# Performance work log

Measured on AMD Instinct MI355X. Metric: run time of the kernel, lower is better.

## Reference

```python
import jax, jax.numpy as jnp
import numpy as np

N_SEQ, BS, E, H = 2048, 8, 512, 8
HD = E // H  # 64


def setup_inputs() -> dict:
    key = jax.random.key(0)
    k1, k2, k3 = jax.random.split(key, 3)
    seq = jax.random.normal(k1, (N_SEQ, BS, E), dtype=jnp.float32)
    # xavier_uniform for Linear(E, 3E): bound = sqrt(6/(fan_in+fan_out))
    b_qkv_w = float(np.sqrt(6.0 / (E + 3 * E)))
    W_qkv = jax.random.uniform(k2, (3 * E, E), minval=-b_qkv_w, maxval=b_qkv_w, dtype=jnp.float32)
    b_out_w = float(np.sqrt(6.0 / (E + E)))
    W_out = jax.random.uniform(k3, (E, E), minval=-b_out_w, maxval=b_out_w, dtype=jnp.float32)
    b_qkv = jnp.zeros((3 * E,), dtype=jnp.float32)
    b_out = jnp.zeros((E,), dtype=jnp.float32)
    return {"seq": seq, "W_qkv": W_qkv, "b_qkv": b_qkv, "W_out": W_out, "b_out": b_out}


def reference(seq, W_qkv, b_qkv, W_out, b_out):
    n, bs, e = seq.shape
    # fused QKV projection: [n, bs, 3E]
    qkv = jnp.einsum('nbe,fe->nbf', seq, W_qkv) + b_qkv
    # [n, bs, 3, H, HD] -> q/k/v each [n, bs*H, HD] (bs outer, H inner)
    qkv = qkv.reshape(n, bs, 3, H, HD)
    q = qkv[:, :, 0].reshape(n, bs * H, HD)
    k = qkv[:, :, 1].reshape(n, bs * H, HD)
    v = qkv[:, :, 2].reshape(n, bs * H, HD)
    scale = 1.0 / jnp.sqrt(jnp.asarray(HD, dtype=seq.dtype))
    # full [bs*H, n, n] score matrix as in the original
    attn = jnp.einsum('qbd,kbd->bqk', q * scale, k)
    attn = jax.nn.softmax(attn, axis=-1)
    out = jnp.einsum('bqk,kbd->qbd', attn, v)  # [n, bs*H, HD]
    out = out.reshape(n, bs, e)
    return jnp.einsum('nbe,fe->nbf', out, W_out) + b_out
```

## Files before the change

kernel.cpp:

```cpp
#include <hip/hip_runtime.h>
#include <stdint.h>

typedef unsigned short ushort_t;
typedef unsigned int uint32;
typedef __attribute__((ext_vector_type(8))) short short8;
typedef __attribute__((ext_vector_type(4))) float f32x4;
typedef __attribute__((ext_vector_type(16))) float f32x16;
typedef __attribute__((ext_vector_type(4))) uint32 uint4v;

#define NSEQ 2048
#define BSZ 8
#define EMB 512
#define NHEAD 8
#define HDIM 64
#define MTOK (NSEQ*BSZ)
#define NH_TOT (BSZ*NHEAD)
#define NT (NSEQ/64)

#define VMCNT0 asm volatile("s_waitcnt vmcnt(0)" ::: "memory")
#define VMCNT4 asm volatile("s_waitcnt vmcnt(4)" ::: "memory")
#define BAR __builtin_amdgcn_s_barrier()

__device__ __forceinline__ ushort_t f2bf(float f) {
  uint32_t u = __builtin_bit_cast(uint32_t, f);
  u += 0x7FFFu + ((u >> 16) & 1u);
  return (ushort_t)(u >> 16);
}
__device__ __forceinline__ float bf2f(ushort_t u) {
  uint32_t x = ((uint32_t)u) << 16;
  return __builtin_bit_cast(float, x);
}

__device__ __forceinline__ void gll16(const void* g, void* l) {
  __builtin_amdgcn_global_load_lds(
      (const __attribute__((address_space(1))) void*)g,
      (__attribute__((address_space(3))) void*)l, 16, 0, 0);
}

__device__ __forceinline__ int SW(int r) { return (r & 7) ^ ((r >> 3) & 7); }

__global__ void cvt_f32_bf16(const float* __restrict__ in, ushort_t* __restrict__ out, int n4) {
  int i = blockIdx.x * blockDim.x + threadIdx.x;
  if (i >= n4) return;
  float4 v = reinterpret_cast<const float4*>(in)[i];
  union { ushort_t u[4]; uint64_t q; } o;
  o.u[0] = f2bf(v.x); o.u[1] = f2bf(v.y); o.u[2] = f2bf(v.z); o.u[3] = f2bf(v.w);
  reinterpret_cast<uint64_t*>(out)[i] = o.q;
}

template<int MODE>
__global__ __launch_bounds__(256) void gemm_bt(
    const ushort_t* __restrict__ A, const ushort_t* __restrict__ B,
    const float* __restrict__ bias,
    float* __restrict__ Cf, ushort_t* __restrict__ Cq,
    int M, int N, int K)
{
  __shared__ __align__(16) ushort_t As[128*64];
  __shared__ __align__(16) ushort_t Bs[128*64];
  const int t = threadIdx.x;
  const int w = t >> 6, l = t & 63;
  const int tm = blockIdx.y * 128, tn = blockIdx.x * 128;
  const int wm = w >> 1, wn = w & 1;

  f32x4 acc[4][4] = {};

  for (int k0 = 0; k0 < K; k0 += 64) {
    #pragma unroll
    for (int j = 0; j < 4; ++j) {
      int row = j*32 + w*8 + (l >> 3);
      int cole = ((l & 7) * 8) ^ ((row & 7) << 3);
      const ushort_t* ga = A + (size_t)(tm + row) * K + k0 + cole;
      const ushort_t* gb = B + (size_t)(tn + row) * K + k0 + cole;
      gll16(ga, As + j*2048 + w*512 + l*8);
      gll16(gb, Bs + j*2048 + w*512 + l*8);
    }
    __syncthreads();
    #pragma unroll
    for (int kk = 0; kk < 2; ++kk) {
      short8 af[4], bfr[4];
      #pragma unroll
      for (int mi = 0; mi < 4; ++mi) {
        int row = wm*64 + mi*16 + (l & 15);
        int byte = row*128 + ((kk*64 + ((l >> 4) * 16)) ^ ((row & 7) << 4));
        af[mi] = *reinterpret_cast<const short8*>(reinterpret_cast<const char*>(As) + byte);
      }
      #pragma unroll
      for (int ni = 0; ni < 4; ++ni) {
        int row = wn*64 + ni*16 + (l & 15);
        int byte = row*128 + ((kk*64 + ((l >> 4) * 16)) ^ ((row & 7) << 4));
        bfr[ni] = *reinterpret_cast<const short8*>(reinterpret_cast<const char*>(Bs) + byte);
      }
      #pragma unroll
      for (int mi = 0; mi < 4; ++mi)
        #pragma unroll
        for (int ni = 0; ni < 4; ++ni)
          acc[mi][ni] = __builtin_amdgcn_mfma_f32_16x16x32_bf16(af[mi], bfr[ni], acc[mi][ni], 0, 0, 0);
    }
    __syncthreads();
  }

  #pragma unroll
  for (int mi = 0; mi < 4; ++mi) {
    #pragma unroll
    for (int ni = 0; ni < 4; ++ni) {
      #pragma unroll
      for (int r = 0; r < 4; ++r) {
        int row = tm + wm*64 + mi*16 + ((l >> 4) * 4) + r;
        int col = tn + wn*64 + ni*16 + (l & 15);
        float v = acc[mi][ni][r] + bias[col];
        if constexpr (MODE == 1) {
          Cf[(size_t)row * N + col] = v;
        } else {
          int w3 = col >> 9, hx = (col >> 6) & 7, hd = col & 63;
          int n = row >> 3, bb = row & 7;
          Cq[(size_t)w3 * ((size_t)NH_TOT * NSEQ * HDIM)
             + ((size_t)(bb * NHEAD + hx) * NSEQ + n) * HDIM + hd] = f2bf(v);
        }
      }
    }
  }
}

__global__ __launch_bounds__(256) void transpose_v(
    const ushort_t* __restrict__ V, ushort_t* __restrict__ VT)
{
  __shared__ __align__(16) ushort_t T[64*64];
  const int t = threadIdx.x;
  const int head = blockIdx.y;
  const int n0 = blockIdx.x * 64;
  const size_t base = (size_t)head * NSEQ * HDIM;
  const int r = t >> 3, c0 = (t & 7) * 8;

  short8 a = *reinterpret_cast<const short8*>(V + base + (size_t)(n0 + r) * HDIM + c0);
  short8 b = *reinterpret_cast<const short8*>(V + base + (size_t)(n0 + r + 32) * HDIM + c0);
  #pragma unroll
  for (int e = 0; e < 8; ++e) {
    int d = c0 + e; int sw = SW(d) << 4;
    *reinterpret_cast<ushort_t*>(reinterpret_cast<char*>(T) + d*128 + ((r*2) ^ sw)) = (ushort_t)a[e];
    *reinterpret_cast<ushort_t*>(reinterpret_cast<char*>(T) + d*128 + (((r+32)*2) ^ sw)) = (ushort_t)b[e];
  }
  __syncthreads();
  #pragma unroll
  for (int i = 0; i < 2; ++i) {
    int d = (t >> 3) + 32*i, ch = t & 7;
    short8 v = *reinterpret_cast<const short8*>(
        reinterpret_cast<const char*>(T) + d*128 + ((ch*16) ^ (SW(d) << 4)));
    *reinterpret_cast<short8*>(VT + (size_t)head * HDIM * NSEQ + (size_t)d * NSEQ + n0 + ch*8) = v;
  }
}

#define CSC 0.18033688011112042f

__global__ __launch_bounds__(256, 3) void attn_fwd(
    const ushort_t* __restrict__ Qb, const ushort_t* __restrict__ Kb,
    const ushort_t* __restrict__ VTb, ushort_t* __restrict__ Ob)
{
  __shared__ __align__(16) ushort_t Ks[3][64*64];
  __shared__ __align__(16) ushort_t Vs[3][64*64];
  const int t = threadIdx.x, w = t >> 6, l = t & 63;
  const int lq = l & 31, h = l >> 5;
  const int L = blockIdx.x + 16 * blockIdx.y;
  const int Tid = (L & 7) * 128 + (L >> 3);
  const int bh = Tid >> 4, qt = Tid & 15;
  const int b = bh >> 3, hh = bh & 7;
  const size_t hbase  = (size_t)bh * NSEQ * HDIM;
  const size_t vtbase = (size_t)bh * HDIM * NSEQ;
  const int qbase = qt*128 + w*32;

  short8 qreg[4];
  #pragma unroll
  for (int kd = 0; kd < 4; ++kd) {
    short8 raw = *reinterpret_cast<const short8*>(
        Qb + hbase + (size_t)(qbase + lq) * HDIM + kd*16 + h*8);
    short8 q;
    #pragma unroll
    for (int e = 0; e < 8; ++e)
      q[e] = (short)f2bf(bf2f((ushort_t)raw[e]) * CSC);
    qreg[kd] = q;
  }

  f32x16 Oacc[2] = {};
  f32x16 lacc = {};

  const short ONE = (short)0x3F80;
  short8 ones = { ONE, ONE, ONE, ONE, ONE, ONE, ONE, ONE };

  const int srow = t >> 3;
  const int scol = (t & 7) * 8;
  const int c0 = scol ^ (SW(srow) << 3);
  const int c1 = scol ^ (SW(srow + 32) << 3);
  const ushort_t* Kg0 = Kb  + hbase  + (size_t)srow       * HDIM + c0;
  const ushort_t* Kg1 = Kb  + hbase  + (size_t)(srow+32)  * HDIM + c1;
  const ushort_t* Vg0 = VTb + vtbase + (size_t)srow       * NSEQ + c0;
  const ushort_t* Vg1 = VTb + vtbase + (size_t)(srow+32)  * NSEQ + c1;

  auto STAGE = [&](int bi, int kt) {
    size_t ko = (size_t)kt * 64 * HDIM;
    int    vo = kt * 64;
    gll16(Kg0 + ko, &Ks[bi][0]    + t*8);
    gll16(Kg1 + ko, &Ks[bi][2048] + t*8);
    gll16(Vg0 + vo, &Vs[bi][0]    + t*8);
    gll16(Vg1 + vo, &Vs[bi][2048] + t*8);
  };

  VMCNT0;
  STAGE(0, 0);
  STAGE(1, 1);

  int cur = 0;
  #pragma unroll 1
  for (int kt = 0; kt < NT; ++kt) {
    if (kt + 1 < NT) { VMCNT4; } else { VMCNT0; }
    BAR;
    if (kt + 2 < NT) {
      int sb = cur + 2; if (sb >= 3) sb -= 3;
      STAGE(sb, kt + 2);
    }

    const char* KsC = reinterpret_cast<const char*>(&Ks[cur][0]);
    const char* VsC = reinterpret_cast<const char*>(&Vs[cur][0]);

    short8 kf[2][4];
    #pragma unroll
    for (int rp = 0; rp < 2; ++rp) {
      int row = rp*32 + lq;
      int swr = SW(row) << 4;
      #pragma unroll
      for (int kd = 0; kd < 4; ++kd)
        kf[rp][kd] = *reinterpret_cast<const short8*>(
            KsC + row*128 + ((kd*32 + h*16) ^ swr));
    }

    f32x16 s0 = {}, s1 = {};
    __builtin_amdgcn_s_setprio(1);
    #pragma unroll
    for (int kd = 0; kd < 4; ++kd) {
      s0 = __builtin_amdgcn_mfma_f32_32x32x16_bf16(kf[0][kd], qreg[kd], s0, 0, 0, 0);
      s1 = __builtin_amdgcn_mfma_f32_32x32x16_bf16(kf[1][kd], qreg[kd], s1, 0, 0, 0);
    }
    __builtin_amdgcn_s_setprio(0);

    short8 vf[2][4];
    #pragma unroll
    for (int dt = 0; dt < 2; ++dt) {
      int d = dt*32 + lq;
      int swd = SW(d) << 4;
      #pragma unroll
      for (int km = 0; km < 4; ++km)
        vf[dt][km] = *reinterpret_cast<const short8*>(
            VsC + d*128 + ((km*32 + h*16) ^ swd));
    }

    #pragma unroll
    for (int r = 0; r < 16; ++r) {
      s0[r] = __builtin_amdgcn_exp2f(s0[r]);
      s1[r] = __builtin_amdgcn_exp2f(s1[r]);
    }

    uint32 w0[8], w1[8];
    #pragma unroll
    for (int i = 0; i < 8; ++i) {
      float a0 = s0[2*i], b0 = s0[2*i+1];
      float a1 = s1[2*i], b1 = s1[2*i+1];
      asm("v_cvt_pk_bf16_f32 %0, %1, %2" : "=v"(w0[i]) : "v"(a0), "v"(b0));
      asm("v_cvt_pk_bf16_f32 %0, %1, %2" : "=v"(w1[i]) : "v"(a1), "v"(b1));
    }
    uint32 pa[4][4];
    #pragma unroll
    for (int sg = 0; sg < 2; ++sg) {
      uint32 a, bb;
      a = w0[4*sg+0]; bb = w0[4*sg+2];
      asm("v_permlane32_swap_b32 %0, %1" : "+v"(a), "+v"(bb));
      pa[sg][0] = a; pa[sg][2] = bb;
      a = w0[4*sg+1]; bb = w0[4*sg+3];
      asm("v_permlane32_swap_b32 %0, %1" : "+v"(a), "+v"(bb));
      pa[sg][1] = a; pa[sg][3] = bb;
      a = w1[4*sg+0]; bb = w1[4*sg+2];
      asm("v_permlane32_swap_b32 %0, %1" : "+v"(a), "+v"(bb));
      pa[2+sg][0] = a; pa[2+sg][2] = bb;
      a = w1[4*sg+1]; bb = w1[4*sg+3];
      asm("v_permlane32_swap_b32 %0, %1" : "+v"(a), "+v"(bb));
      pa[2+sg][1] = a; pa[2+sg][3] = bb;
    }

    __builtin_amdgcn_s_setprio(1);
    #pragma unroll
    for (int km = 0; km < 4; ++km) {
      uint4v u; u[0] = pa[km][0]; u[1] = pa[km][1]; u[2] = pa[km][2]; u[3] = pa[km][3];
      short8 paf = __builtin_bit_cast(short8, u);
      Oacc[0] = __builtin_amdgcn_mfma_f32_32x32x16_bf16(paf, vf[0][km], Oacc[0], 0, 0, 0);
      Oacc[1] = __builtin_amdgcn_mfma_f32_32x32x16_bf16(paf, vf[1][km], Oacc[1], 0, 0, 0);
      lacc    = __builtin_amdgcn_mfma_f32_32x32x16_bf16(paf, ones,     lacc,    0, 0, 0);
    }
    __builtin_amdgcn_s_setprio(0);

    cur = cur + 1; if (cur >= 3) cur = 0;
  }

  #pragma unroll
  for (int r = 0; r < 16; ++r) {
    float li = __builtin_amdgcn_rcpf(lacc[r]);
    int qrow = (r & 3) + 8*(r >> 2) + 4*h;
    int n = qbase + qrow;
    #pragma unroll
    for (int dt = 0; dt < 2; ++dt) {
      int d = dt*32 + lq;
      Ob[((size_t)n * BSZ + b) * EMB + hh*64 + d] = f2bf(Oacc[dt][r] * li);
    }
  }
}

extern "C" void kernel_launch(void* const* d_in, const int* in_sizes, int n_in,
                              void* d_out, int out_size, void* d_ws, size_t ws_size,
                              hipStream_t stream) {
  (void)in_sizes; (void)n_in; (void)out_size; (void)ws_size;
  const float* seq  = (const float*)d_in[0];
  const float* Wqkv = (const float*)d_in[1];
  const float* bqkv = (const float*)d_in[2];
  const float* Wout = (const float*)d_in[3];
  const float* bout = (const float*)d_in[4];
  float* out = (float*)d_out;

  ushort_t* seq_bf  = (ushort_t*)d_ws;
  ushort_t* wqkv_bf = seq_bf  + (size_t)MTOK * EMB;
  ushort_t* wout_bf = wqkv_bf + (size_t)3 * EMB * EMB;
  ushort_t* qkvbuf  = wout_bf + (size_t)EMB * EMB;
  ushort_t* vtbuf   = qkvbuf  + (size_t)3 * NH_TOT * NSEQ * HDIM;
  ushort_t* attno   = qkvbuf  + (size_t)2 * NH_TOT * NSEQ * HDIM;

  cvt_f32_bf16<<<(MTOK*EMB/4 + 255)/256, 256, 0, stream>>>(seq, seq_bf, MTOK*EMB/4);
  cvt_f32_bf16<<<(3*EMB*EMB/4 + 255)/256, 256, 0, stream>>>(Wqkv, wqkv_bf, 3*EMB*EMB/4);
  cvt_f32_bf16<<<(EMB*EMB/4 + 255)/256, 256, 0, stream>>>(Wout, wout_bf, EMB*EMB/4);

  gemm_bt<0><<<dim3(12, 128), 256, 0, stream>>>(seq_bf, wqkv_bf, bqkv, nullptr, qkvbuf,
                                                MTOK, 3*EMB, EMB);

  const ushort_t* Qb  = qkvbuf;
  const ushort_t* Kb  = qkvbuf + (size_t)NH_TOT * NSEQ * HDIM;
  const ushort_t* Vb  = Kb     + (size_t)NH_TOT * NSEQ * HDIM;

  transpose_v<<<dim3(32, 64), 256, 0, stream>>>(Vb, vtbuf);

  attn_fwd<<<dim3(16, 64), 256, 0, stream>>>(Qb, Kb, vtbuf, attno);

  gemm_bt<1><<<dim3(4, 128), 256, 0, stream>>>(attno, wout_bf, bout, out, nullptr,
                                               MTOK, EMB, EMB);
}
```

Measured before the change: 173.5 us.

## Process two query sub-tiles per wave in attention and fuse conversion kernels

Each attention wave now handles 64 query rows (two 32-row sub-tiles) instead of 32, so each K/V tile loaded into LDS and registers is reused twice, and the grid is halved. The row-sum is computed with VALU reductions and a lane shuffle instead of an extra MFMA against a ones vector. The three fp32-to-bf16 conversion launches are merged into one kernel. The cost is higher register pressure, with launch bounds lowered from 3 to 2 blocks per SM, and fewer blocks to fill the GPU.

Measured after the change: 159.3 us. 8.2% less time.

```diff
diff --git a/kernel.cpp b/kernel.cpp
--- a/kernel.cpp
+++ b/kernel.cpp
@@ -5,6 +5,8 @@
 typedef unsigned int uint32;
 typedef __attribute__((ext_vector_type(8))) short short8;
 typedef __attribute__((ext_vector_type(4))) float f32x4;
+typedef __attribute__((ext_vector_type(8))) float f32x8;
+typedef __attribute__((ext_vector_type(2))) float f32x2;
 typedef __attribute__((ext_vector_type(16))) float f32x16;
 typedef __attribute__((ext_vector_type(4))) uint32 uint4v;
 
@@ -39,13 +41,32 @@
 
 __device__ __forceinline__ int SW(int r) { return (r & 7) ^ ((r >> 3) & 7); }
 
-__global__ void cvt_f32_bf16(const float* __restrict__ in, ushort_t* __restrict__ out, int n4) {
+__device__ __forceinline__ float vsum32(f32x16 a, f32x16 b) {
+  f32x16 s = a + b;
+  f32x8 t8 = __builtin_shufflevector(s, s, 0,1,2,3,4,5,6,7)
+           + __builtin_shufflevector(s, s, 8,9,10,11,12,13,14,15);
+  f32x4 t4 = __builtin_shufflevector(t8, t8, 0,1,2,3)
+           + __builtin_shufflevector(t8, t8, 4,5,6,7);
+  f32x2 t2 = __builtin_shufflevector(t4, t4, 0,1)
+           + __builtin_shufflevector(t4, t4, 2,3);
+  return t2[0] + t2[1];
+}
+
+__global__ void cvt3(const float* __restrict__ a, ushort_t* __restrict__ oa, int na4,
+                     const float* __restrict__ b, ushort_t* __restrict__ ob, int nb4,
+                     const float* __restrict__ c, ushort_t* __restrict__ oc, int nc4) {
   int i = blockIdx.x * blockDim.x + threadIdx.x;
-  if (i >= n4) return;
-  float4 v = reinterpret_cast<const float4*>(in)[i];
+  const float* src; ushort_t* dst; int j = i;
+  if (j < na4) { src = a; dst = oa; }
+  else {
+    j -= na4;
+    if (j < nb4) { src = b; dst = ob; }
+    else { j -= nb4; if (j >= nc4) return; src = c; dst = oc; }
+  }
+  float4 v = reinterpret_cast<const float4*>(src)[j];
   union { ushort_t u[4]; uint64_t q; } o;
   o.u[0] = f2bf(v.x); o.u[1] = f2bf(v.y); o.u[2] = f2bf(v.z); o.u[3] = f2bf(v.w);
-  reinterpret_cast<uint64_t*>(out)[i] = o.q;
+  reinterpret_cast<uint64_t*>(dst)[j] = o.q;
 }
 
 template<int MODE>
@@ -151,7 +172,7 @@
 
 #define CSC 0.18033688011112042f
 
-__global__ __launch_bounds__(256, 3) void attn_fwd(
+__global__ __launch_bounds__(256, 2) void attn_fwd(
     const ushort_t* __restrict__ Qb, const ushort_t* __restrict__ Kb,
     const ushort_t* __restrict__ VTb, ushort_t* __restrict__ Ob)
 {
@@ -159,31 +180,30 @@
   __shared__ __align__(16) ushort_t Vs[3][64*64];
   const int t = threadIdx.x, w = t >> 6, l = t & 63;
   const int lq = l & 31, h = l >> 5;
-  const int L = blockIdx.x + 16 * blockIdx.y;
-  const int Tid = (L & 7) * 128 + (L >> 3);
-  const int bh = Tid >> 4, qt = Tid & 15;
+  const int L = blockIdx.x + 8 * blockIdx.y;
+  const int Tid = (L & 7) * 64 + (L >> 3);
+  const int bh = Tid >> 3, qt = Tid & 7;
   const int b = bh >> 3, hh = bh & 7;
   const size_t hbase  = (size_t)bh * NSEQ * HDIM;
   const size_t vtbase = (size_t)bh * HDIM * NSEQ;
-  const int qbase = qt*128 + w*32;
-
-  short8 qreg[4];
+  const int qbase = qt*256 + w*64;
+
+  short8 qreg[2][4];
   #pragma unroll
-  for (int kd = 0; kd < 4; ++kd) {
-    short8 raw = *reinterpret_cast<const short8*>(
-        Qb + hbase + (size_t)(qbase + lq) * HDIM + kd*16 + h*8);
-    short8 q;
-    #pragma unroll
-    for (int e = 0; e < 8; ++e)
-      q[e] = (short)f2bf(bf2f((ushort_t)raw[e]) * CSC);
-    qreg[kd] = q;
-  }
-
-  f32x16 Oacc[2] = {};
-  f32x16 lacc = {};
-
-  const short ONE = (short)0x3F80;
-  short8 ones = { ONE, ONE, ONE, ONE, ONE, ONE, ONE, ONE };
+  for (int qb = 0; qb < 2; ++qb)
+    #pragma unroll
+    for (int kd = 0; kd < 4; ++kd) {
+      short8 raw = *reinterpret_cast<const short8*>(
+          Qb + hbase + (size_t)(qbase + qb*32 + lq) * HDIM + kd*16 + h*8);
+      short8 q;
+      #pragma unroll
+      for (int e = 0; e < 8; ++e)
+        q[e] = (short)f2bf(bf2f((ushort_t)raw[e]) * CSC);
+      qreg[qb][kd] = q;
+    }
+
+  f32x16 Oacc[2][2] = {};
+  float l_run0 = 0.f, l_run1 = 0.f;
 
   const int srow = t >> 3;
   const int scol = (t & 7) * 8;
@@ -231,14 +251,93 @@
             KsC + row*128 + ((kd*32 + h*16) ^ swr));
     }
 
-    f32x16 s0 = {}, s1 = {};
-    __builtin_amdgcn_s_setprio(1);
-    #pragma unroll
-    for (int kd = 0; kd < 4; ++kd) {
-      s0 = __builtin_amdgcn_mfma_f32_32x32x16_bf16(kf[0][kd], qreg[kd], s0, 0, 0, 0);
-      s1 = __builtin_amdgcn_mfma_f32_32x32x16_bf16(kf[1][kd], qreg[kd], s1, 0, 0, 0);
-    }
-    __builtin_amdgcn_s_setprio(0);
+    uint32 pa0[4][4], pa1[4][4];
+
+    {
+      f32x16 s0 = {}, s1 = {};
+      __builtin_amdgcn_s_setprio(1);
+      #pragma unroll
+      for (int kd = 0; kd < 4; ++kd) {
+        s0 = __builtin_amdgcn_mfma_f32_32x32x16_bf16(kf[0][kd], qreg[0][kd], s0, 0, 0, 0);
+        s1 = __builtin_amdgcn_mfma_f32_32x32x16_bf16(kf[1][kd], qreg[0][kd], s1, 0, 0, 0);
+      }
+      __builtin_amdgcn_s_setprio(0);
+      #pragma unroll
+      for (int r = 0; r < 16; ++r) {
+        s0[r] = __builtin_amdgcn_exp2f(s0[r]);
+        s1[r] = __builtin_amdgcn_exp2f(s1[r]);
+      }
+      float ps = vsum32(s0, s1);
+      ps += __shfl_xor(ps, 32);
+      l_run0 += ps;
+      uint32 w0[8], w1[8];
+      #pragma unroll
+      for (int i = 0; i < 8; ++i) {
+        float a0 = s0[2*i], b0 = s0[2*i+1];
+        float a1 = s1[2*i], b1 = s1[2*i+1];
+        asm("v_cvt_pk_bf16_f32 %0, %1, %2" : "=v"(w0[i]) : "v"(a0), "v"(b0));
+        asm("v_cvt_pk_bf16_f32 %0, %1, %2" : "=v"(w1[i]) : "v"(a1), "v"(b1));
+      }
+      #pragma unroll
+      for (int sg = 0; sg < 2; ++sg) {
+        uint32 a, bb;
+        a = w0[4*sg+0]; bb = w0[4*sg+2];
+        asm("v_permlane32_swap_b32 %0, %1" : "+v"(a), "+v"(bb));
+        pa0[sg][0] = a; pa0[sg][2] = bb;
+        a = w0[4*sg+1]; bb = w0[4*sg+3];
+        asm("v_permlane32_swap_b32 %0, %1" : "+v"(a), "+v"(bb));
+        pa0[sg][1] = a; pa0[sg][3] = bb;
+        a = w1[4*sg+0]; bb = w1[4*sg+2];
+        asm("v_permlane32_swap_b32 %0, %1" : "+v"(a), "+v"(bb));
+        pa0[2+sg][0] = a; pa0[2+sg][2] = bb;
+        a = w1[4*sg+1]; bb = w1[4*sg+3];
+        asm("v_permlane32_swap_b32 %0, %1" : "+v"(a), "+v"(bb));
+        pa0[2+sg][1] = a; pa0[2+sg][3] = bb;
+      }
+    }
+
+    {
+      f32x16 s0 = {}, s1 = {};
+      __builtin_amdgcn_s_setprio(1);
+      #pragma unroll
+      for (int kd = 0; kd < 4; ++kd) {
+        s0 = __builtin_amdgcn_mfma_f32_32x32x16_bf16(kf[0][kd], qreg[1][kd], s0, 0, 0, 0);
+        s1 = __builtin_amdgcn_mfma_f32_32x32x16_bf16(kf[1][kd], qreg[1][kd], s1, 0, 0, 0);
+      }
+      __builtin_amdgcn_s_setprio(0);
+      #pragma unroll
+      for (int r = 0; r < 16; ++r) {
+        s0[r] = __builtin_amdgcn_exp2f(s0[r]);
+        s1[r] = __builtin_amdgcn_exp2f(s1[r]);
+      }
+      float ps = vsum32(s0, s1);
+      ps += __shfl_xor(ps, 32);
+      l_run1 += ps;
+      uint32 w0[8], w1[8];
+      #pragma unroll
+      for (int i = 0; i < 8; ++i) {
+        float a0 = s0[2*i], b0 = s0[2*i+1];
+        float a1 = s1[2*i], b1 = s1[2*i+1];
+        asm("v_cvt_pk_bf16_f32 %0, %1, %2" : "=v"(w0[i]) : "v"(a0), "v"(b0));
+        asm("v_cvt_pk_bf16_f32 %0, %1, %2" : "=v"(w1[i]) : "v"(a1), "v"(b1));
+      }
+      #pragma unroll
+      for (int sg = 0; sg < 2; ++sg) {
+        uint32 a, bb;
+        a = w0[4*sg+0]; bb = w0[4*sg+2];
+        asm("v_permlane32_swap_b32 %0, %1" : "+v"(a), "+v"(bb));
+        pa1[sg][0] = a; pa1[sg][2] = bb;
+        a = w0[4*sg+1]; bb = w0[4*sg+3];
+        asm("v_permlane32_swap_b32 %0, %1" : "+v"(a), "+v"(bb));
+        pa1[sg][1] = a; pa1[sg][3] = bb;
+        a = w1[4*sg+0]; bb = w1[4*sg+2];
+        asm("v_permlane32_swap_b32 %0, %1" : "+v"(a), "+v"(bb));
+        pa1[2+sg][0] = a; pa1[2+sg][2] = bb;
+        a = w1[4*sg+1]; bb = w1[4*sg+3];
+        asm("v_permlane32_swap_b32 %0, %1" : "+v"(a), "+v"(bb));
+        pa1[2+sg][1] = a; pa1[2+sg][3] = bb;
+      }
+    }
 
     short8 vf[2][4];
     #pragma unroll
@@ -251,61 +350,37 @@
             VsC + d*128 + ((km*32 + h*16) ^ swd));
     }
 
-    #pragma unroll
-    for (int r = 0; r < 16; ++r) {
-      s0[r] = __builtin_amdgcn_exp2f(s0[r]);
-      s1[r] = __builtin_amdgcn_exp2f(s1[r]);
-    }
-
-    uint32 w0[8], w1[8];
-    #pragma unroll
-    for (int i = 0; i < 8; ++i) {
-      float a0 = s0[2*i], b0 = s0[2*i+1];
-      float a1 = s1[2*i], b1 = s1[2*i+1];
-      asm("v_cvt_pk_bf16_f32 %0, %1, %2" : "=v"(w0[i]) : "v"(a0), "v"(b0));
-      asm("v_cvt_pk_bf16_f32 %0, %1, %2" : "=v"(w1[i]) : "v"(a1), "v"(b1));
-    }
-    uint32 pa[4][4];
-    #pragma unroll
-    for (int sg = 0; sg < 2; ++sg) {
-      uint32 a, bb;
-      a = w0[4*sg+0]; bb = w0[4*sg+2];
-      asm("v_permlane32_swap_b32 %0, %1" : "+v"(a), "+v"(bb));
-      pa[sg][0] = a; pa[sg][2] = bb;
-      a = w0[4*sg+1]; bb = w0[4*sg+3];
-      asm("v_permlane32_swap_b32 %0, %1" : "+v"(a), "+v"(bb));
-      pa[sg][1] = a; pa[sg][3] = bb;
-      a = w1[4*sg+0]; bb = w1[4*sg+2];
-      asm("v_permlane32_swap_b32 %0, %1" : "+v"(a), "+v"(bb));
-      pa[2+sg][0] = a; pa[2+sg][2] = bb;
-      a = w1[4*sg+1]; bb = w1[4*sg+3];
-      asm("v_permlane32_swap_b32 %0, %1" : "+v"(a), "+v"(bb));
-      pa[2+sg][1] = a; pa[2+sg][3] = bb;
-    }
-
     __builtin_amdgcn_s_setprio(1);
     #pragma unroll
     for (int km = 0; km < 4; ++km) {
-      uint4v u; u[0] = pa[km][0]; u[1] = pa[km][1]; u[2] = pa[km][2]; u[3] = pa[km][3];
-      short8 paf = __builtin_bit_cast(short8, u);
-      Oacc[0] = __builtin_amdgcn_mfma_f32_32x32x16_bf16(paf, vf[0][km], Oacc[0], 0, 0, 0);
-      Oacc[1] = __builtin_amdgcn_mfma_f32_32x32x16_bf16(paf, vf[1][km], Oacc[1], 0, 0, 0);
-      lacc    = __builtin_amdgcn_mfma_f32_32x32x16_bf16(paf, ones,     lacc,    0, 0, 0);
+      uint4v u0; u0[0] = pa0[km][0]; u0[1] = pa0[km][1]; u0[2] = pa0[km][2]; u0[3] = pa0[km][3];
+      short8 paf0 = __builtin_bit_cast(short8, u0);
+      uint4v u1; u1[0] = pa1[km][0]; u1[1] = pa1[km][1]; u1[2] = pa1[km][2]; u1[3] = pa1[km][3];
+      short8 paf1 = __builtin_bit_cast(short8, u1);
+      Oacc[0][0] = __builtin_amdgcn_mfma_f32_32x32x16_bf16(paf0, vf[0][km], Oacc[0][0], 0, 0, 0);
+      Oacc[0][1] = __builtin_amdgcn_mfma_f32_32x32x16_bf16(paf0, vf[1][km], Oacc[0][1], 0, 0, 0);
+      Oacc[1][0] = __builtin_amdgcn_mfma_f32_32x32x16_bf16(paf1, vf[0][km], Oacc[1][0], 0, 0, 0);
+      Oacc[1][1] = __builtin_amdgcn_mfma_f32_32x32x16_bf16(paf1, vf[1][km], Oacc[1][1], 0, 0, 0);
     }
     __builtin_amdgcn_s_setprio(0);
 
     cur = cur + 1; if (cur >= 3) cur = 0;
   }
 
+  float linv0 = __builtin_amdgcn_rcpf(l_run0);
+  float linv1 = __builtin_amdgcn_rcpf(l_run1);
   #pragma unroll
   for (int r = 0; r < 16; ++r) {
-    float li = __builtin_amdgcn_rcpf(lacc[r]);
     int qrow = (r & 3) + 8*(r >> 2) + 4*h;
-    int n = qbase + qrow;
+    float li0 = __shfl(linv0, qrow, 64);
+    float li1 = __shfl(linv1, qrow, 64);
     #pragma unroll
     for (int dt = 0; dt < 2; ++dt) {
       int d = dt*32 + lq;
-      Ob[((size_t)n * BSZ + b) * EMB + hh*64 + d] = f2bf(Oacc[dt][r] * li);
+      int n0 = qbase + qrow;
+      int n1 = qbase + 32 + qrow;
+      Ob[((size_t)n0 * BSZ + b) * EMB + hh*64 + d] = f2bf(Oacc[0][dt][r] * li0);
+      Ob[((size_t)n1 * BSZ + b) * EMB + hh*64 + d] = f2bf(Oacc[1][dt][r] * li1);
     }
   }
 }
@@ -328,9 +403,9 @@
   ushort_t* vtbuf   = qkvbuf  + (size_t)3 * NH_TOT * NSEQ * HDIM;
   ushort_t* attno   = qkvbuf  + (size_t)2 * NH_TOT * NSEQ * HDIM;
 
-  cvt_f32_bf16<<<(MTOK*EMB/4 + 255)/256, 256, 0, stream>>>(seq, seq_bf, MTOK*EMB/4);
-  cvt_f32_bf16<<<(3*EMB*EMB/4 + 255)/256, 256, 0, stream>>>(Wqkv, wqkv_bf, 3*EMB*EMB/4);
-  cvt_f32_bf16<<<(EMB*EMB/4 + 255)/256, 256, 0, stream>>>(Wout, wout_bf, EMB*EMB/4);
+  const int na4 = MTOK*EMB/4, nb4 = 3*EMB*EMB/4, nc4 = EMB*EMB/4;
+  cvt3<<<(na4+nb4+nc4 + 255)/256, 256, 0, stream>>>(
+      seq, seq_bf, na4, Wqkv, wqkv_bf, nb4, Wout, wout_bf, nc4);
 
   gemm_bt<0><<<dim3(12, 128), 256, 0, stream>>>(seq_bf, wqkv_bf, bqkv, nullptr, qkvbuf,
                                                 MTOK, 3*EMB, EMB);
@@ -341,7 +416,7 @@
 
   transpose_v<<<dim3(32, 64), 256, 0, stream>>>(Vb, vtbuf);
 
-  attn_fwd<<<dim3(16, 64), 256, 0, stream>>>(Qb, Kb, vtbuf, attno);
+  attn_fwd<<<dim3(8, 64), 256, 0, stream>>>(Qb, Kb, vtbuf, attno);
 
   gemm_bt<1><<<dim3(4, 128), 256, 0, stream>>>(attno, wout_bf, bout, out, nullptr,
                                                MTOK, EMB, EMB);
```

## Drop ones-MFMA row sum, double-buffer attention LDS, fuse conversion kernels

Applied to the files above, without the earlier changes.

In the attention kernel, the row-sum MFMA against a ones vector is replaced by a VALU/shuffle reduction of the exponentiated scores, accumulated as a scalar and broadcast per row at the end. The LDS ring shrinks from triple to double buffering with an extra barrier per iteration, and launch bounds rise to 4 blocks per CU to raise occupancy. The V fragment loads move later to shorten register live ranges, and the three f32->bf16 conversion launches are merged into one. This trades MFMA work and LDS footprint for extra VALU reductions, cross-lane shuffles and a second barrier per tile, which reduces latency hiding.

Result: faster. 165.5 us (-4.6%).

```diff
diff --git a/kernel.cpp b/kernel.cpp
--- a/kernel.cpp
+++ b/kernel.cpp
@@ -5,6 +5,8 @@
 typedef unsigned int uint32;
 typedef __attribute__((ext_vector_type(8))) short short8;
 typedef __attribute__((ext_vector_type(4))) float f32x4;
+typedef __attribute__((ext_vector_type(8))) float f32x8;
+typedef __attribute__((ext_vector_type(2))) float f32x2;
 typedef __attribute__((ext_vector_type(16))) float f32x16;
 typedef __attribute__((ext_vector_type(4))) uint32 uint4v;
 
@@ -39,13 +41,32 @@
 
 __device__ __forceinline__ int SW(int r) { return (r & 7) ^ ((r >> 3) & 7); }
 
-__global__ void cvt_f32_bf16(const float* __restrict__ in, ushort_t* __restrict__ out, int n4) {
+__device__ __forceinline__ float vsum32(f32x16 a, f32x16 b) {
+  f32x16 s = a + b;
+  f32x8 t8 = __builtin_shufflevector(s, s, 0,1,2,3,4,5,6,7)
+           + __builtin_shufflevector(s, s, 8,9,10,11,12,13,14,15);
+  f32x4 t4 = __builtin_shufflevector(t8, t8, 0,1,2,3)
+           + __builtin_shufflevector(t8, t8, 4,5,6,7);
+  f32x2 t2 = __builtin_shufflevector(t4, t4, 0,1)
+           + __builtin_shufflevector(t4, t4, 2,3);
+  return t2[0] + t2[1];
+}
+
+__global__ void cvt3(const float* __restrict__ a, ushort_t* __restrict__ oa, int na4,
+                     const float* __restrict__ b, ushort_t* __restrict__ ob, int nb4,
+                     const float* __restrict__ c, ushort_t* __restrict__ oc, int nc4) {
   int i = blockIdx.x * blockDim.x + threadIdx.x;
-  if (i >= n4) return;
-  float4 v = reinterpret_cast<const float4*>(in)[i];
+  const float* src; ushort_t* dst; int j = i;
+  if (j < na4) { src = a; dst = oa; }
+  else {
+    j -= na4;
+    if (j < nb4) { src = b; dst = ob; }
+    else { j -= nb4; if (j >= nc4) return; src = c; dst = oc; }
+  }
+  float4 v = reinterpret_cast<const float4*>(src)[j];
   union { ushort_t u[4]; uint64_t q; } o;
   o.u[0] = f2bf(v.x); o.u[1] = f2bf(v.y); o.u[2] = f2bf(v.z); o.u[3] = f2bf(v.w);
-  reinterpret_cast<uint64_t*>(out)[i] = o.q;
+  reinterpret_cast<uint64_t*>(dst)[j] = o.q;
 }
 
 template<int MODE>
@@ -151,12 +172,12 @@
 
 #define CSC 0.18033688011112042f
 
-__global__ __launch_bounds__(256, 3) void attn_fwd(
+__global__ __launch_bounds__(256, 4) void attn_fwd(
     const ushort_t* __restrict__ Qb, const ushort_t* __restrict__ Kb,
     const ushort_t* __restrict__ VTb, ushort_t* __restrict__ Ob)
 {
-  __shared__ __align__(16) ushort_t Ks[3][64*64];
-  __shared__ __align__(16) ushort_t Vs[3][64*64];
+  __shared__ __align__(16) ushort_t Ks[2][64*64];
+  __shared__ __align__(16) ushort_t Vs[2][64*64];
   const int t = threadIdx.x, w = t >> 6, l = t & 63;
   const int lq = l & 31, h = l >> 5;
   const int L = blockIdx.x + 16 * blockIdx.y;
@@ -180,10 +201,7 @@
   }
 
   f32x16 Oacc[2] = {};
-  f32x16 lacc = {};
-
-  const short ONE = (short)0x3F80;
-  short8 ones = { ONE, ONE, ONE, ONE, ONE, ONE, ONE, ONE };
+  float l_run = 0.f;
 
   const int srow = t >> 3;
   const int scol = (t & 7) * 8;
@@ -205,17 +223,13 @@
 
   VMCNT0;
   STAGE(0, 0);
-  STAGE(1, 1);
 
   int cur = 0;
   #pragma unroll 1
   for (int kt = 0; kt < NT; ++kt) {
-    if (kt + 1 < NT) { VMCNT4; } else { VMCNT0; }
+    if (kt + 1 < NT) { STAGE(cur ^ 1, kt + 1); VMCNT4; }
+    else             { VMCNT0; }
     BAR;
-    if (kt + 2 < NT) {
-      int sb = cur + 2; if (sb >= 3) sb -= 3;
-      STAGE(sb, kt + 2);
-    }
 
     const char* KsC = reinterpret_cast<const char*>(&Ks[cur][0]);
     const char* VsC = reinterpret_cast<const char*>(&Vs[cur][0]);
@@ -240,22 +254,14 @@
     }
     __builtin_amdgcn_s_setprio(0);
 
-    short8 vf[2][4];
-    #pragma unroll
-    for (int dt = 0; dt < 2; ++dt) {
-      int d = dt*32 + lq;
-      int swd = SW(d) << 4;
-      #pragma unroll
-      for (int km = 0; km < 4; ++km)
-        vf[dt][km] = *reinterpret_cast<const short8*>(
-            VsC + d*128 + ((km*32 + h*16) ^ swd));
-    }
-
     #pragma unroll
     for (int r = 0; r < 16; ++r) {
       s0[r] = __builtin_amdgcn_exp2f(s0[r]);
       s1[r] = __builtin_amdgcn_exp2f(s1[r]);
     }
+    float ps = vsum32(s0, s1);
+    ps += __shfl_xor(ps, 32);
+    l_run += ps;
 
     uint32 w0[8], w1[8];
     #pragma unroll
@@ -265,42 +271,46 @@
       asm("v_cvt_pk_bf16_f32 %0, %1, %2" : "=v"(w0[i]) : "v"(a0), "v"(b0));
       asm("v_cvt_pk_bf16_f32 %0, %1, %2" : "=v"(w1[i]) : "v"(a1), "v"(b1));
     }
-    uint32 pa[4][4];
-    #pragma unroll
-    for (int sg = 0; sg < 2; ++sg) {
-      uint32 a, bb;
-      a = w0[4*sg+0]; bb = w0[4*sg+2];
-      asm("v_permlane32_swap_b32 %0, %1" : "+v"(a), "+v"(bb));
-      pa[sg][0] = a; pa[sg][2] = bb;
-      a = w0[4*sg+1]; bb = w0[4*sg+3];
-      asm("v_permlane32_swap_b32 %0, %1" : "+v"(a), "+v"(bb));
-      pa[sg][1] = a; pa[sg][3] = bb;
-      a = w1[4*sg+0]; bb = w1[4*sg+2];
-      asm("v_permlane32_swap_b32 %0, %1" : "+v"(a), "+v"(bb));
-      pa[2+sg][0] = a; pa[2+sg][2] = bb;
-      a = w1[4*sg+1]; bb = w1[4*sg+3];
-      asm("v_permlane32_swap_b32 %0, %1" : "+v"(a), "+v"(bb));
-      pa[2+sg][1] = a; pa[2+sg][3] = bb;
+
+    short8 vf[2][4];
+    #pragma unroll
+    for (int dt = 0; dt < 2; ++dt) {
+      int d = dt*32 + lq;
+      int swd = SW(d) << 4;
+      #pragma unroll
+      for (int km = 0; km < 4; ++km)
+        vf[dt][km] = *reinterpret_cast<const short8*>(
+            VsC + d*128 + ((km*32 + h*16) ^ swd));
     }
 
     __builtin_amdgcn_s_setprio(1);
     #pragma unroll
-    for (int km = 0; km < 4; ++km) {
-      uint4v u; u[0] = pa[km][0]; u[1] = pa[km][1]; u[2] = pa[km][2]; u[3] = pa[km][3];
-      short8 paf = __builtin_bit_cast(short8, u);
-      Oacc[0] = __builtin_amdgcn_mfma_f32_32x32x16_bf16(paf, vf[0][km], Oacc[0], 0, 0, 0);
-      Oacc[1] = __builtin_amdgcn_mfma_f32_32x32x16_bf16(paf, vf[1][km], Oacc[1], 0, 0, 0);
-      lacc    = __builtin_amdgcn_mfma_f32_32x32x16_bf16(paf, ones,     lacc,    0, 0, 0);
+    for (int half = 0; half < 2; ++half) {
+      #pragma unroll
+      for (int sg = 0; sg < 2; ++sg) {
+        int km = half*2 + sg;
+        uint32 a, bb, c, d;
+        if (half == 0) { a = w0[4*sg+0]; bb = w0[4*sg+2]; c = w0[4*sg+1]; d = w0[4*sg+3]; }
+        else           { a = w1[4*sg+0]; bb = w1[4*sg+2]; c = w1[4*sg+1]; d = w1[4*sg+3]; }
+        asm("v_permlane32_swap_b32 %0, %1" : "+v"(a), "+v"(bb));
+        asm("v_permlane32_swap_b32 %0, %1" : "+v"(c), "+v"(d));
+        uint4v u; u[0] = a; u[1] = c; u[2] = bb; u[3] = d;
+        short8 paf = __builtin_bit_cast(short8, u);
+        Oacc[0] = __builtin_amdgcn_mfma_f32_32x32x16_bf16(paf, vf[0][km], Oacc[0], 0, 0, 0);
+        Oacc[1] = __builtin_amdgcn_mfma_f32_32x32x16_bf16(paf, vf[1][km], Oacc[1], 0, 0, 0);
+      }
     }
     __builtin_amdgcn_s_setprio(0);
 
-    cur = cur + 1; if (cur >= 3) cur = 0;
-  }
-
+    BAR;
+    cur ^= 1;
+  }
+
+  float linv = __builtin_amdgcn_rcpf(l_run);
   #pragma unroll
   for (int r = 0; r < 16; ++r) {
-    float li = __builtin_amdgcn_rcpf(lacc[r]);
     int qrow = (r & 3) + 8*(r >> 2) + 4*h;
+    float li = __shfl(linv, qrow, 64);
     int n = qbase + qrow;
     #pragma unroll
     for (int dt = 0; dt < 2; ++dt) {
@@ -328,9 +338,9 @@
   ushort_t* vtbuf   = qkvbuf  + (size_t)3 * NH_TOT * NSEQ * HDIM;
   ushort_t* attno   = qkvbuf  + (size_t)2 * NH_TOT * NSEQ * HDIM;
 
-  cvt_f32_bf16<<<(MTOK*EMB/4 + 255)/256, 256, 0, stream>>>(seq, seq_bf, MTOK*EMB/4);
-  cvt_f32_bf16<<<(3*EMB*EMB/4 + 255)/256, 256, 0, stream>>>(Wqkv, wqkv_bf, 3*EMB*EMB/4);
-  cvt_f32_bf16<<<(EMB*EMB/4 + 255)/256, 256, 0, stream>>>(Wout, wout_bf, EMB*EMB/4);
+  const int na4 = MTOK*EMB/4, nb4 = 3*EMB*EMB/4, nc4 = EMB*EMB/4;
+  cvt3<<<(na4+nb4+nc4 + 255)/256, 256, 0, stream>>>(
+      seq, seq_bf, na4, Wqkv, wqkv_bf, nb4, Wout, wout_bf, nc4);
 
   gemm_bt<0><<<dim3(12, 128), 256, 0, stream>>>(seq_bf, wqkv_bf, bqkv, nullptr, qkvbuf,
                                                 MTOK, 3*EMB, EMB);
```
